# Kernel optimization log

Measured on AMD Instinct MI355X. Metric: run time of the kernel, lower is better.

## Reference

```python
import jax, jax.numpy as jnp
import numpy as np

SHIFT = 1  # fixed shift_direction (module draws +/-1 at random; we pin +1)

def setup_inputs() -> dict:
    key = jax.random.key(0)
    kx, kw = jax.random.split(key)
    x = jax.random.normal(kx, (1024, 256, 7, 7), dtype=jnp.float32)
    W = jax.random.normal(kw, (128, 3, 3, 512), dtype=jnp.float32)
    return {"x": x, "W": W}

def _fwd(x, W):
    B = x.shape[0]
    t = x.reshape(B, 256, 7, 7)
    # unfold((3,1), padding=(1,0)) along H: t[b,c,k,h,w] = x_pad[b,c,h+k-1,w]
    xp = jnp.pad(t, ((0, 0), (0, 0), (1, 1), (0, 0)))
    t = jnp.stack([xp[:, :, k:k + 7, :] for k in range(3)], axis=2)  # (B,256,3,7,7)
    t = t.reshape(B, 2, 128, 3, 7, 7).transpose(0, 2, 3, 4, 1, 5)   # (B,128,3,7,2,7)
    t = t.reshape(B, 128, 3, 14, 7)
    t = jnp.roll(t, SHIFT, axis=3)
    t = t.reshape(B, 128, 3, 7, 2, 7).sum(axis=4)                   # (B,128,3,7,7)
    t = t.transpose(0, 1, 3, 2, 4)                                  # (B,128,7,3,7)
    t = jnp.roll(t, SHIFT, axis=4)
    # second unfold((3,1), padding=(1,0)) along W dim: gather 3 shifted slices
    tp = jnp.pad(t, ((0, 0), (0, 0), (0, 0), (0, 0), (1, 1)))
    t3 = jnp.stack([tp[..., k2:k2 + 7] for k2 in range(3)], axis=-1)  # (B,128,7,3,7,3) = (m,l,n,j,o,k)
    out = jnp.einsum('mlnjok,ljki->mnoi', t3, W)                     # (B,7,7,512)
    return out.transpose(0, 3, 1, 2)                                 # (B,512,7,7)

def reference(x, W):
    return _fwd(x, W)
```

## Files before the change

kernel.cpp:

```cpp
#include <hip/hip_runtime.h>

typedef __attribute__((ext_vector_type(8)))  __bf16 bvec8;
typedef __attribute__((ext_vector_type(4)))  __bf16 bvec4;
typedef __attribute__((ext_vector_type(16))) float  fvec16;
typedef __attribute__((ext_vector_type(8)))  short  svec8;

__device__ __forceinline__ void gload16(const void* g, void* l) {
    __builtin_amdgcn_global_load_lds(
        (const __attribute__((address_space(1))) void*)g,
        (__attribute__((address_space(3))) void*)l,
        16, 0, 0);
}

__global__ __launch_bounds__(256) void pack_w(const float* __restrict__ W,
                                              __bf16* __restrict__ Wp) {
    int u = blockIdx.x * 256 + threadIdx.x;
    if (u >= 73728) return;
    int lane = u & 63;
    int it2  = (u >> 6) & 15;
    int kt16 = u >> 10;
    int i  = it2 * 32 + (lane & 31);
    int K0 = kt16 * 16 + ((lane >> 5) << 3);
    bvec8 o;
#pragma unroll
    for (int e = 0; e < 8; ++e) {
        int K  = K0 + e;
        int jk = K >> 7;
        int l  = K & 127;
        int j  = (jk * 11) >> 5;
        int k  = jk - 3 * j;
        o[e] = (__bf16)W[((l * 9 + j * 3 + k) << 9) + i];
    }
    *(bvec8*)&Wp[(size_t)u * 8] = o;
}

__global__ __launch_bounds__(512, 4) void conv_mfma(
    const float* __restrict__ x, const __bf16* __restrict__ Wp,
    float* __restrict__ out)
{
    extern __shared__ char smem[];
    __bf16* ys = (__bf16*)smem;
    char*  reg2 = smem + 37888;
    __bf16* xs  = (__bf16*)reg2;

    const int tid  = threadIdx.x;
    const int lane = tid & 63;
    const int l31  = lane & 31;
    const int ls5  = lane >> 5;
    const int wv   = tid >> 6;
    const int b    = blockIdx.x;

    const float* xb = x + (size_t)b * 12544;
    const char*  WpB = (const char*)Wp;

    for (int it = 0; it < 7; ++it) {
        int e4 = it * 512 + tid;
        if (e4 < 3136) {
            const float4 v = ((const float4*)xb)[e4];
            bvec4 pk = { (__bf16)v.x, (__bf16)v.y, (__bf16)v.z, (__bf16)v.w };
            *(bvec4*)&xs[e4 * 4] = pk;
        }
    }
    __syncthreads();

    for (int it = 0; it < 5; ++it) {
        int up = it * 512 + tid;
        if (up < 2368) {
            int row  = up >> 4;
            int useg = up & 15;
            bvec8 ov;
            if (row >= 147) {
                ov = __builtin_bit_cast(bvec8, (svec8)0);
                row = 147;
            } else {
                int w   = row % 7;
                int njq = row / 7;
                int j   = njq % 3;
                int n   = njq / 3;
                int rA  = n + j - 1;
                bool mA = (unsigned)rA < 7u;
                int rB  = n + j + 5; if (rB >= 7) rB -= 7; if (rB >= 7) rB -= 7;
                bool mB = !((j == 0 && n == 1) || (j == 2 && n == 0));
                int cA  = rA * 7 + w;
                int cB  = rB * 7 + w;
                int l0  = useg * 8;
#pragma unroll
                for (int d = 0; d < 8; ++d) {
                    float fa = mA ? (float)xs[(l0 + d) * 49 + cA] : 0.f;
                    float fb = mB ? (float)xs[(128 + l0 + d) * 49 + cB] : 0.f;
                    ov[d] = (__bf16)(fa + fb);
                }
            }
            *(bvec8*)&ys[(row << 7) + ((useg ^ (row & 15)) << 3)] = ov;
        }
    }

    int nn21[2], oo[2];
#pragma unroll
    for (int sn = 0; sn < 2; ++sn) {
        int s = sn * 32 + l31;
        int sc = (s < 49) ? s : 48;
        int n = sc / 7;
        nn21[sn] = n * 21;
        oo[sn]   = sc - n * 7;
    }

    fvec16 acc[2][2];
#pragma unroll
    for (int am = 0; am < 2; ++am)
#pragma unroll
        for (int sn = 0; sn < 2; ++sn)
#pragma unroll
            for (int r = 0; r < 16; ++r) acc[am][sn][r] = 0.f;

    __syncthreads();

    {
        const char* g0 = WpB + (tid << 4);
        char* d0 = reg2 + (tid << 4);
        gload16(g0, d0);
        gload16(g0 + 8192, d0 + 8192);
        gload16(g0 + 16384, d0 + 16384);
        gload16(g0 + 24576, d0 + 24576);
    }
    __syncthreads();

    for (int jk = 0; jk < 9; ++jk) {
        const int j = (jk * 11) >> 5;
        const int k = jk - 3 * j;
        int rowB[2], rx[2];
#pragma unroll
        for (int sn = 0; sn < 2; ++sn) {
            int o  = oo[sn];
            int tw = o + k + 5;
            int w  = tw >= 7 ? tw - 7 : tw;
            int row = nn21[sn] + j * 7 + w;
            if ((k == 0 && o == 0) || (k == 2 && o == 6)) row = 147;
            rowB[sn] = row << 7;
            rx[sn]   = row & 15;
        }
#pragma unroll
        for (int q = 0; q < 8; ++q) {
            const int kt = jk * 8 + q;
            if (kt) __syncthreads();
            if (kt && kt + 1 < 72) {
                const char* g = WpB + ((size_t)(kt + 1) << 14) + (tid << 4);
                char* d = reg2 + (((kt + 1) & 1) << 14) + (tid << 4);
                gload16(g, d);
                gload16(g + 8192, d + 8192);
            }
            const __bf16* ws = (const __bf16*)(reg2 + ((kt & 1) << 14));
            bvec8 wf[2], bf[2];
#pragma unroll
            for (int am = 0; am < 2; ++am)
                wf[am] = *(const bvec8*)&ws[((wv * 2 + am) << 9) + (lane << 3)];
#pragma unroll
            for (int sn = 0; sn < 2; ++sn) {
                int u = ((q << 1) + ls5) ^ rx[sn];
                bf[sn] = *(const bvec8*)&ys[rowB[sn] + (u << 3)];
            }
            __builtin_amdgcn_s_setprio(1);
            acc[0][0] = __builtin_amdgcn_mfma_f32_32x32x16_bf16(wf[0], bf[0], acc[0][0], 0, 0, 0);
            acc[0][1] = __builtin_amdgcn_mfma_f32_32x32x16_bf16(wf[0], bf[1], acc[0][1], 0, 0, 0);
            acc[1][0] = __builtin_amdgcn_mfma_f32_32x32x16_bf16(wf[1], bf[0], acc[1][0], 0, 0, 0);
            acc[1][1] = __builtin_amdgcn_mfma_f32_32x32x16_bf16(wf[1], bf[1], acc[1][1], 0, 0, 0);
            __builtin_amdgcn_s_setprio(0);
        }
    }

    const size_t obase = (size_t)b * 25088;
#pragma unroll
    for (int am = 0; am < 2; ++am) {
        const int i0 = (wv * 2 + am) * 32 + 4 * ls5;
#pragma unroll
        for (int sn = 0; sn < 2; ++sn) {
            const int s = sn * 32 + l31;
            if (sn == 1 && l31 >= 17) continue;
#pragma unroll
            for (int r = 0; r < 16; ++r) {
                int i = i0 + (r & 3) + 8 * (r >> 2);
                out[obase + (size_t)i * 49 + s] = acc[am][sn][r];
            }
        }
    }
}

extern "C" void kernel_launch(void* const* d_in, const int* in_sizes, int n_in,
                              void* d_out, int out_size, void* d_ws, size_t ws_size,
                              hipStream_t stream) {
    const float* x = (const float*)d_in[0];
    const float* W = (const float*)d_in[1];
    float* out = (float*)d_out;
    __bf16* Wp = (__bf16*)d_ws;
    (void)in_sizes; (void)n_in; (void)out_size; (void)ws_size;

    hipFuncSetAttribute(reinterpret_cast<const void*>(conv_mfma),
                        hipFuncAttributeMaxDynamicSharedMemorySize, 70656);

    hipLaunchKernelGGL(pack_w, dim3(288), dim3(256), 0, stream, W, Wp);
    hipLaunchKernelGGL(conv_mfma, dim3(1024), dim3(512), 70656, stream, x, Wp, out);
}
```

Baseline: 109.6 us.

## Load weight fragments directly to registers and split output channels across two blocks

Weight fragments now go straight from global memory into registers with a software-prefetched double buffer, so the weight tiles no longer pass through LDS and the per-step __syncthreads barriers disappear. Each batch sample is split across two blocks, each covering half of the output channels, with waves split over channel and spatial tiles; the grid doubles. In exchange, the x-to-bf16 conversion and the y construction in LDS are repeated in both blocks. Each wave's global weight loads must now hide their own latency behind the MFMA work without any LDS staging.

```diff
diff --git a/kernel.cpp b/kernel.cpp
--- a/kernel.cpp
+++ b/kernel.cpp
@@ -4,13 +4,6 @@
 typedef __attribute__((ext_vector_type(4)))  __bf16 bvec4;
 typedef __attribute__((ext_vector_type(16))) float  fvec16;
 typedef __attribute__((ext_vector_type(8)))  short  svec8;
-
-__device__ __forceinline__ void gload16(const void* g, void* l) {
-    __builtin_amdgcn_global_load_lds(
-        (const __attribute__((address_space(1))) void*)g,
-        (__attribute__((address_space(3))) void*)l,
-        16, 0, 0);
-}
 
 __global__ __launch_bounds__(256) void pack_w(const float* __restrict__ W,
                                               __bf16* __restrict__ Wp) {
@@ -38,20 +31,36 @@
     const float* __restrict__ x, const __bf16* __restrict__ Wp,
     float* __restrict__ out)
 {
-    extern __shared__ char smem[];
-    __bf16* ys = (__bf16*)smem;
-    char*  reg2 = smem + 37888;
-    __bf16* xs  = (__bf16*)reg2;
+    __shared__ __bf16 xs[12544];
+    __shared__ __bf16 ys[148 * 128];
 
     const int tid  = threadIdx.x;
     const int lane = tid & 63;
     const int l31  = lane & 31;
     const int ls5  = lane >> 5;
-    const int wv   = tid >> 6;
-    const int b    = blockIdx.x;
+    const int wid  = tid >> 6;
+    const int wi   = wid & 3;
+    const int wsn  = wid >> 2;
+    const int bx   = blockIdx.x;
+    const int b    = bx >> 1;
+    const int ih   = bx & 1;
 
     const float* xb = x + (size_t)b * 12544;
     const char*  WpB = (const char*)Wp;
+    const int it2b = ih * 8 + wi * 2;
+
+    bvec8 aE[2][2], aO[2][2];
+    {
+        const char* g = WpB + ((size_t)lane << 4);
+#pragma unroll
+        for (int am = 0; am < 2; ++am)
+#pragma unroll
+            for (int h = 0; h < 2; ++h) {
+                const int unit = h * 16 + it2b + am;
+                aE[am][h] = *(const bvec8*)(g + (unit << 10));
+                aO[am][h] = *(const bvec8*)(g + 32768 + (unit << 10));
+            }
+    }
 
     for (int it = 0; it < 7; ++it) {
         int e4 = it * 512 + tid;
@@ -95,91 +104,88 @@
         }
     }
 
-    int nn21[2], oo[2];
-#pragma unroll
-    for (int sn = 0; sn < 2; ++sn) {
-        int s = sn * 32 + l31;
-        int sc = (s < 49) ? s : 48;
-        int n = sc / 7;
-        nn21[sn] = n * 21;
-        oo[sn]   = sc - n * 7;
-    }
-
-    fvec16 acc[2][2];
+    const int s_  = wsn * 32 + l31;
+    const int sc  = (s_ < 49) ? s_ : 48;
+    const int nq  = sc / 7;
+    const int nn21 = nq * 21;
+    const int oo   = sc - nq * 7;
+
+    fvec16 acc[2];
 #pragma unroll
     for (int am = 0; am < 2; ++am)
 #pragma unroll
-        for (int sn = 0; sn < 2; ++sn)
-#pragma unroll
-            for (int r = 0; r < 16; ++r) acc[am][sn][r] = 0.f;
+        for (int r = 0; r < 16; ++r) acc[am][r] = 0.f;
 
     __syncthreads();
 
-    {
-        const char* g0 = WpB + (tid << 4);
-        char* d0 = reg2 + (tid << 4);
-        gload16(g0, d0);
-        gload16(g0 + 8192, d0 + 8192);
-        gload16(g0 + 16384, d0 + 16384);
-        gload16(g0 + 24576, d0 + 24576);
-    }
-    __syncthreads();
+#define GEO(JK, ROWE, RX) {                                                   \
+        int j_ = ((JK) * 11) >> 5; int k_ = (JK) - 3 * j_;                    \
+        int tw_ = oo + k_ + 5; int w_ = tw_ >= 7 ? tw_ - 7 : tw_;             \
+        int row_ = nn21 + j_ * 7 + w_;                                        \
+        if ((k_ == 0 && oo == 0) || (k_ == 2 && oo == 6)) row_ = 147;         \
+        ROWE = row_ << 7; RX = row_ & 15; }
+
+#define READF(BUF, P, ROWE, RX) {                                             \
+        _Pragma("unroll")                                                     \
+        for (int h = 0; h < 2; ++h) {                                         \
+            int u_ = ((P) * 4 + h * 2 + ls5) ^ (RX);                          \
+            BUF[h] = *(const bvec8*)&ys[(ROWE) + (u_ << 3)]; } }
+
+#define MFMA4(BUF, AW) {                                                      \
+        __builtin_amdgcn_s_setprio(1);                                        \
+        _Pragma("unroll")                                                     \
+        for (int h = 0; h < 2; ++h)                                           \
+        _Pragma("unroll")                                                     \
+        for (int am = 0; am < 2; ++am)                                        \
+            acc[am] = __builtin_amdgcn_mfma_f32_32x32x16_bf16(                \
+                AW[am][h], BUF[h], acc[am], 0, 0, 0);                         \
+        __builtin_amdgcn_s_setprio(0); }
+
+#define PREFW(AW, T) if ((T) < 36) {                                          \
+        const char* gp = WpB + ((size_t)(T) << 15) + ((size_t)lane << 4);     \
+        _Pragma("unroll")                                                     \
+        for (int am = 0; am < 2; ++am)                                        \
+        _Pragma("unroll")                                                     \
+        for (int h = 0; h < 2; ++h)                                           \
+            AW[am][h] = *(const bvec8*)(gp + ((h * 16 + it2b + am) << 10)); }
+
+    int rowE, rx, rowEn, rxn;
+    GEO(0, rowE, rx);
+    bvec8 bufA[2], bufB[2];
+    READF(bufA, 0, rowE, rx);
 
     for (int jk = 0; jk < 9; ++jk) {
-        const int j = (jk * 11) >> 5;
-        const int k = jk - 3 * j;
-        int rowB[2], rx[2];
-#pragma unroll
-        for (int sn = 0; sn < 2; ++sn) {
-            int o  = oo[sn];
-            int tw = o + k + 5;
-            int w  = tw >= 7 ? tw - 7 : tw;
-            int row = nn21[sn] + j * 7 + w;
-            if ((k == 0 && o == 0) || (k == 2 && o == 6)) row = 147;
-            rowB[sn] = row << 7;
-            rx[sn]   = row & 15;
-        }
-#pragma unroll
-        for (int q = 0; q < 8; ++q) {
-            const int kt = jk * 8 + q;
-            if (kt) __syncthreads();
-            if (kt && kt + 1 < 72) {
-                const char* g = WpB + ((size_t)(kt + 1) << 14) + (tid << 4);
-                char* d = reg2 + (((kt + 1) & 1) << 14) + (tid << 4);
-                gload16(g, d);
-                gload16(g + 8192, d + 8192);
-            }
-            const __bf16* ws = (const __bf16*)(reg2 + ((kt & 1) << 14));
-            bvec8 wf[2], bf[2];
-#pragma unroll
-            for (int am = 0; am < 2; ++am)
-                wf[am] = *(const bvec8*)&ws[((wv * 2 + am) << 9) + (lane << 3)];
-#pragma unroll
-            for (int sn = 0; sn < 2; ++sn) {
-                int u = ((q << 1) + ls5) ^ rx[sn];
-                bf[sn] = *(const bvec8*)&ys[rowB[sn] + (u << 3)];
-            }
-            __builtin_amdgcn_s_setprio(1);
-            acc[0][0] = __builtin_amdgcn_mfma_f32_32x32x16_bf16(wf[0], bf[0], acc[0][0], 0, 0, 0);
-            acc[0][1] = __builtin_amdgcn_mfma_f32_32x32x16_bf16(wf[0], bf[1], acc[0][1], 0, 0, 0);
-            acc[1][0] = __builtin_amdgcn_mfma_f32_32x32x16_bf16(wf[1], bf[0], acc[1][0], 0, 0, 0);
-            acc[1][1] = __builtin_amdgcn_mfma_f32_32x32x16_bf16(wf[1], bf[1], acc[1][1], 0, 0, 0);
-            __builtin_amdgcn_s_setprio(0);
-        }
-    }
+        const int t0 = jk * 4;
+        READF(bufB, 1, rowE, rx);
+        MFMA4(bufA, aE);
+        PREFW(aE, t0 + 2);
+        READF(bufA, 2, rowE, rx);
+        MFMA4(bufB, aO);
+        PREFW(aO, t0 + 3);
+        READF(bufB, 3, rowE, rx);
+        { int jn = jk < 8 ? jk + 1 : 8; GEO(jn, rowEn, rxn); }
+        MFMA4(bufA, aE);
+        PREFW(aE, t0 + 4);
+        READF(bufA, 0, rowEn, rxn);
+        MFMA4(bufB, aO);
+        PREFW(aO, t0 + 5);
+        rowE = rowEn; rx = rxn;
+    }
+
+#undef GEO
+#undef READF
+#undef MFMA4
+#undef PREFW
 
     const size_t obase = (size_t)b * 25088;
-#pragma unroll
-    for (int am = 0; am < 2; ++am) {
-        const int i0 = (wv * 2 + am) * 32 + 4 * ls5;
-#pragma unroll
-        for (int sn = 0; sn < 2; ++sn) {
-            const int s = sn * 32 + l31;
-            if (sn == 1 && l31 >= 17) continue;
+    if (!(wsn == 1 && l31 >= 17)) {
+#pragma unroll
+        for (int am = 0; am < 2; ++am) {
+            const int i0 = ih * 256 + (wi * 2 + am) * 32 + 4 * ls5;
 #pragma unroll
             for (int r = 0; r < 16; ++r) {
                 int i = i0 + (r & 3) + 8 * (r >> 2);
-                out[obase + (size_t)i * 49 + s] = acc[am][sn][r];
+                out[obase + (size_t)i * 49 + s_] = acc[am][r];
             }
         }
     }
@@ -194,9 +200,6 @@
     __bf16* Wp = (__bf16*)d_ws;
     (void)in_sizes; (void)n_in; (void)out_size; (void)ws_size;
 
-    hipFuncSetAttribute(reinterpret_cast<const void*>(conv_mfma),
-                        hipFuncAttributeMaxDynamicSharedMemorySize, 70656);
-
     hipLaunchKernelGGL(pack_w, dim3(288), dim3(256), 0, stream, W, Wp);
-    hipLaunchKernelGGL(conv_mfma, dim3(1024), dim3(512), 70656, stream, x, Wp, out);
+    hipLaunchKernelGGL(conv_mfma, dim3(2048), dim3(512), 0, stream, x, Wp, out);
 }
```

Result: slower. 121.8 us (+11.2%).
